# Performance work log

Hardware: AMD Instinct MI355X
Metric: run time of the kernel (lower is better)

Reference implementation:

```python
import jax, jax.numpy as jnp
import numpy as np

EMBED = 1024
HEADS = 16
HEAD_DIM = EMBED // HEADS


def setup_inputs() -> dict:
    key = jax.random.key(0)
    ks = jax.random.split(key, 9)
    s = 0.02
    return {
        "hidden_states": jax.random.normal(ks[0], (1, 4, 1500, EMBED), dtype=jnp.float32),
        "q_w": jax.random.normal(ks[1], (EMBED, EMBED), dtype=jnp.float32) * s,
        "q_b": jax.random.normal(ks[2], (EMBED,), dtype=jnp.float32) * s,
        "k_w": jax.random.normal(ks[3], (EMBED, EMBED), dtype=jnp.float32) * s,
        "v_w": jax.random.normal(ks[4], (EMBED, EMBED), dtype=jnp.float32) * s,
        "v_b": jax.random.normal(ks[5], (EMBED,), dtype=jnp.float32) * s,
        "out_w": jax.random.normal(ks[6], (EMBED, EMBED), dtype=jnp.float32) * s,
        "out_b": jax.random.normal(ks[7], (EMBED,), dtype=jnp.float32) * s,
    }


def reference(hidden_states, q_w, q_b, k_w, v_w, v_b, out_w, out_b):
    # hidden_states: [1, B, S, E]
    _, bsz, tgt_len, _ = hidden_states.shape
    x = hidden_states[0]  # [B, S, E]
    scaling = HEAD_DIM ** -0.5

    def split_heads(t):  # [B, S, E] -> [B, H, S, Dh]
        return t.reshape(bsz, tgt_len, HEADS, HEAD_DIM).transpose(0, 2, 1, 3)

    # Linear layers use torch convention: y = x @ W.T + b  (k_proj has no bias)
    q = split_heads((x @ q_w.T + q_b) * scaling)
    k = split_heads(x @ k_w.T)
    v = split_heads(x @ v_w.T + v_b)

    # attention scores [B, H, S, S]
    attn_weights = jnp.einsum("bhqd,bhkd->bhqk", q, k)
    attn_probs = jax.nn.softmax(attn_weights, axis=-1)
    attn_out = jnp.einsum("bhqk,bhkd->bhqd", attn_probs, v)  # [B, H, S, Dh]

    attn_out = attn_out.transpose(0, 2, 1, 3).reshape(1, bsz, tgt_len, EMBED)
    return attn_out @ out_w.T + out_b
```

## Files before the change

kernel.cpp:

```cpp
#include <hip/hip_runtime.h>
#include <cstddef>
#include <cstdint>

#define EMB 1024
#define SEQ 1500
#define NB 4
#define NH 16
#define DH 64
#define MTOT (NB*SEQ)
#define VTS 1536

typedef __bf16 bf16;
typedef __bf16 bf16x4 __attribute__((ext_vector_type(4)));
typedef __bf16 bf16x8 __attribute__((ext_vector_type(8)));
typedef short  s16x4  __attribute__((ext_vector_type(4)));
typedef float  f32x4  __attribute__((ext_vector_type(4)));

#define LOG2E 1.44269504088896340736f

__device__ __forceinline__ void async16(const void* g, const void* l) {
    __builtin_amdgcn_global_load_lds(
        (const __attribute__((address_space(1))) uint32_t*)g,
        (__attribute__((address_space(3))) uint32_t*)l, 16, 0, 0);
}

__device__ __forceinline__ uint32_t pack_bf16_trunc(float e0, float e1) {
    return __builtin_amdgcn_perm(__builtin_bit_cast(uint32_t, e1),
                                 __builtin_bit_cast(uint32_t, e0), 0x07060302u);
}

struct CvtArgs {
    const float* xs; bf16* xd;
    const float* w[4]; bf16* wd[4];
};

__global__ __launch_bounds__(256) void cvt_kernel(CvtArgs a) {
    const size_t NX = (size_t)MTOT * EMB;
    const size_t NW = (size_t)EMB * EMB;
    const size_t tot = NX + 4 * NW;
    for (size_t i = ((size_t)blockIdx.x * 256 + threadIdx.x) * 4; i < tot;
         i += (size_t)gridDim.x * 1024) {
        const float* s; bf16* d; size_t off;
        if (i < NX) { s = a.xs; d = a.xd; off = i; }
        else {
            size_t j = i - NX;
            int wi = (int)(j >> 20);
            off = j & (NW - 1);
            s = a.w[wi]; d = a.wd[wi];
        }
        float4 v = *(const float4*)(s + off);
        bf16x4 o = { (bf16)v.x, (bf16)v.y, (bf16)v.z, (bf16)v.w };
        *(bf16x4*)(d + off) = o;
    }
}

__global__ __launch_bounds__(256, 3) void gemm_fused(
    const bf16* __restrict__ X,
    const bf16* __restrict__ W0, const bf16* __restrict__ W1, const bf16* __restrict__ W2,
    const float* __restrict__ b_q, const float* __restrict__ b_v,
    bf16* __restrict__ Oq, bf16* __restrict__ Ok, bf16* __restrict__ Ovt,
    int M)
{
    __shared__ bf16 A0s[2][128 * 32];
    __shared__ bf16 A1s[2][128 * 32];
    __shared__ bf16 Bs [2][128 * 32];
    const int tid = threadIdx.x;
    const int lane = tid & 63, w = tid >> 6;
    const int q = lane >> 4, lr = lane & 15;
    const int wr = w >> 1, wc = w & 1;

    const int id = blockIdx.x;
    const bool isV = id >= 384;
    const int vid = isV ? id - 384 : id;
    const int mtile = (vid & 7) + ((vid >> 3) % 6) * 8;
    const int ntile = (vid >> 3) / 6;
    const int m0 = mtile * 128, n0 = ntile * 128;

    const int srow = w * 32 + (lane >> 2);
    const int swz_ch = (((lane & 3) ^ ((lane >> 3) & 3))) * 8;

    const bf16* pA0[2]; const bf16* pB[2];
    const size_t WOFF = (size_t)(W1 - W0);
#pragma unroll
    for (int i = 0; i < 2; i++) {
        int mr = m0 + srow + i * 16; mr = mr < M ? mr : M - 1;
        int nr = n0 + srow + i * 16;
        if (!isV) {
            pA0[i] = W0 + (size_t)nr * EMB + swz_ch;
            pB[i]  = X  + (size_t)mr * EMB + swz_ch;
        } else {
            pA0[i] = X  + (size_t)mr * EMB + swz_ch;
            pB[i]  = W2 + (size_t)nr * EMB + swz_ch;
        }
    }

#define STAGE(buf, off) do { \
    async16(pA0[0] + (off), A0s[buf] + (w * 2 + 0) * 512); \
    async16(pA0[1] + (off), A0s[buf] + (w * 2 + 1) * 512); \
    async16(pB[0]  + (off), Bs[buf]  + (w * 2 + 0) * 512); \
    async16(pB[1]  + (off), Bs[buf]  + (w * 2 + 1) * 512); \
    if (!isV) { \
        async16(pA0[0] + WOFF + (off), A1s[buf] + (w * 2 + 0) * 512); \
        async16(pA0[1] + WOFF + (off), A1s[buf] + (w * 2 + 1) * 512); } \
    } while (0)

    STAGE(0, 0);

    f32x4 acc0[4][4] = {};
    f32x4 acc1[4][4] = {};
    const int qsw = (q ^ ((lr >> 1) & 3)) * 8;
    const int arow = (wr * 64 + lr) * 32;
    const int brow = (wc * 64 + lr) * 32;

    for (int k0 = 0; k0 < EMB; k0 += 32) {
        const int cur = (k0 >> 5) & 1;
        __syncthreads();
        const int nxt = k0 + 32;
        if (nxt < EMB) STAGE(cur ^ 1, nxt);

        bf16x8 af[4], bfr[4];
#pragma unroll
        for (int t = 0; t < 4; t++) {
            bfr[t] = *(const bf16x8*)(Bs[cur]  + brow + t * 512 + qsw);
            af[t]  = *(const bf16x8*)(A0s[cur] + arow + t * 512 + qsw);
        }
#pragma unroll
        for (int ti = 0; ti < 4; ti++)
#pragma unroll
            for (int tj = 0; tj < 4; tj++)
                acc0[ti][tj] = __builtin_amdgcn_mfma_f32_16x16x32_bf16(
                    af[ti], bfr[tj], acc0[ti][tj], 0, 0, 0);
        if (!isV) {
#pragma unroll
            for (int t = 0; t < 4; t++)
                af[t] = *(const bf16x8*)(A1s[cur] + arow + t * 512 + qsw);
#pragma unroll
            for (int ti = 0; ti < 4; ti++)
#pragma unroll
                for (int tj = 0; tj < 4; tj++)
                    acc1[ti][tj] = __builtin_amdgcn_mfma_f32_16x16x32_bf16(
                        af[ti], bfr[tj], acc1[ti][tj], 0, 0, 0);
        }
    }
#undef STAGE

    if (!isV) {
        const float scale = 0.125f * LOG2E;
#pragma unroll
        for (int tj = 0; tj < 4; tj++) {
            const int m = m0 + wc * 64 + tj * 16 + lr;
            if (m >= M) continue;
            const int b_ = m / SEQ, s_ = m % SEQ;
#pragma unroll
            for (int ti = 0; ti < 4; ti++) {
                const int nb = n0 + wr * 64 + ti * 16 + q * 4;
                const int h = nb >> 6, d = nb & 63;
                const size_t ooff = (((size_t)b_ * NH + h) * SEQ + s_) * DH + d;
                const float4 b4 = *(const float4*)(b_q + nb);
                bf16x4 oq, ok;
                oq[0] = (bf16)((acc0[ti][tj][0] + b4.x) * scale);
                oq[1] = (bf16)((acc0[ti][tj][1] + b4.y) * scale);
                oq[2] = (bf16)((acc0[ti][tj][2] + b4.z) * scale);
                oq[3] = (bf16)((acc0[ti][tj][3] + b4.w) * scale);
                ok[0] = (bf16)(acc1[ti][tj][0]);
                ok[1] = (bf16)(acc1[ti][tj][1]);
                ok[2] = (bf16)(acc1[ti][tj][2]);
                ok[3] = (bf16)(acc1[ti][tj][3]);
                *(bf16x4*)(Oq + ooff) = oq;
                *(bf16x4*)(Ok + ooff) = ok;
            }
        }
    } else {
#pragma unroll
        for (int ti = 0; ti < 4; ti++) {
            const int mb = m0 + wr * 64 + ti * 16 + q * 4;
            if (mb >= M) continue;
            const int b_ = mb / SEQ, s_ = mb % SEQ;
#pragma unroll
            for (int tj = 0; tj < 4; tj++) {
                const int nb = n0 + wc * 64 + tj * 16 + lr;
                const int h = nb >> 6, d = nb & 63;
                const float bv = b_v[nb];
                bf16x4 o;
                o[0] = (bf16)(acc0[ti][tj][0] + bv);
                o[1] = (bf16)(acc0[ti][tj][1] + bv);
                o[2] = (bf16)(acc0[ti][tj][2] + bv);
                o[3] = (bf16)(acc0[ti][tj][3] + bv);
                *(bf16x4*)(Ovt + ((size_t)(b_ * NH + h) * DH + d) * VTS + s_) = o;
            }
        }
    }
}

__global__ __launch_bounds__(256) void gemm_out(
    const bf16* __restrict__ X, const bf16* __restrict__ Wo,
    const float* __restrict__ b_o, float* __restrict__ Of, int M)
{
    __shared__ bf16 As[2][128 * 32];
    __shared__ bf16 Bs[2][128 * 32];
    const int tid = threadIdx.x;
    const int lane = tid & 63, w = tid >> 6;
    const int q = lane >> 4, lr = lane & 15;
    const int wr = w >> 1, wc = w & 1;

    const int id = blockIdx.x;
    const int mtile = (id & 7) + ((id >> 3) % 6) * 8;
    const int ntile = (id >> 3) / 6;
    const int m0 = mtile * 128, n0 = ntile * 128;

    const int srow = w * 32 + (lane >> 2);
    const int swz_ch = (((lane & 3) ^ ((lane >> 3) & 3))) * 8;
    const bf16* pA[2]; const bf16* pB[2];
#pragma unroll
    for (int i = 0; i < 2; i++) {
        int ra = n0 + srow + i * 16;
        int rb = m0 + srow + i * 16; rb = rb < M ? rb : M - 1;
        pA[i] = Wo + (size_t)ra * EMB + swz_ch;
        pB[i] = X + (size_t)rb * EMB + swz_ch;
    }

#pragma unroll
    for (int i = 0; i < 2; i++) {
        async16(pA[i], As[0] + (w * 2 + i) * 512);
        async16(pB[i], Bs[0] + (w * 2 + i) * 512);
    }

    f32x4 acc[4][4] = {};
    const int qsw = (q ^ ((lr >> 1) & 3)) * 8;
    const int arow = (wr * 64 + lr) * 32;
    const int brow = (wc * 64 + lr) * 32;

    for (int k0 = 0; k0 < EMB; k0 += 32) {
        const int cur = (k0 >> 5) & 1;
        __syncthreads();
        const int nxt = k0 + 32;
        if (nxt < EMB) {
#pragma unroll
            for (int i = 0; i < 2; i++) {
                async16(pA[i] + nxt, As[cur ^ 1] + (w * 2 + i) * 512);
                async16(pB[i] + nxt, Bs[cur ^ 1] + (w * 2 + i) * 512);
            }
        }
        bf16x8 af[4], bfr[4];
#pragma unroll
        for (int t = 0; t < 4; t++) {
            af[t]  = *(const bf16x8*)(As[cur] + arow + t * 512 + qsw);
            bfr[t] = *(const bf16x8*)(Bs[cur] + brow + t * 512 + qsw);
        }
#pragma unroll
        for (int ti = 0; ti < 4; ti++)
#pragma unroll
            for (int tj = 0; tj < 4; tj++)
                acc[ti][tj] = __builtin_amdgcn_mfma_f32_16x16x32_bf16(
                    af[ti], bfr[tj], acc[ti][tj], 0, 0, 0);
    }

#pragma unroll
    for (int tj = 0; tj < 4; tj++) {
        const int m = m0 + wc * 64 + tj * 16 + lr;
        if (m >= M) continue;
#pragma unroll
        for (int ti = 0; ti < 4; ti++) {
            const int nb = n0 + wr * 64 + ti * 16 + q * 4;
            const float4 b4 = *(const float4*)(b_o + nb);
            float4 o;
            o.x = acc[ti][tj][0] + b4.x;
            o.y = acc[ti][tj][1] + b4.y;
            o.z = acc[ti][tj][2] + b4.z;
            o.w = acc[ti][tj][3] + b4.w;
            *(float4*)(Of + (size_t)m * EMB + nb) = o;
        }
    }
}

#define QG 3
__global__ __launch_bounds__(256) void attn_mfma(
    const bf16* __restrict__ Qb, const bf16* __restrict__ Kb,
    const bf16* __restrict__ Vt, bf16* __restrict__ ctx)
{
    __shared__ bf16 Ks[2][64 * 64];
    __shared__ bf16 Vs[2][64 * 64];
    const int tid = threadIdx.x;
    const int lane = tid & 63, w = tid >> 6;
    const int q = lane >> 4, lr = lane & 15;
    const int bh = blockIdx.x, b_ = bh >> 4, h_ = bh & 15;
    const int q0 = blockIdx.y * (QG * 64);
    const size_t base = (size_t)bh * SEQ * DH;
    const size_t vbase = (size_t)bh * DH * VTS;

    int qrow[QG];
    bf16x8 qf[QG][2];
#pragma unroll
    for (int g = 0; g < QG; g++) {
        qrow[g] = q0 + g * 64 + w * 16 + lr;
        const int qrc = qrow[g] < SEQ ? qrow[g] : (SEQ - 1);
        qf[g][0] = *(const bf16x8*)(Qb + base + (size_t)qrc * DH + q * 8);
        qf[g][1] = *(const bf16x8*)(Qb + base + (size_t)qrc * DH + 32 + q * 8);
    }

    f32x4 oacc[QG][4] = {};
    f32x4 lacc[QG] = {};
    const s16x4 ones = { (short)0x3F80, (short)0x3F80, (short)0x3F80, (short)0x3F80 };

    const int srow = tid >> 3;
    const int sch8 = ((tid & 7) ^ (srow & 7)) * 8;
    const int kswz = lr & 7;

    const int NT = (SEQ + 63) / 64;

    {
        int r0 = srow, r1 = srow + 32;
        async16(Kb + base + (size_t)r0 * DH + sch8, Ks[0] + tid * 8);
        async16(Kb + base + (size_t)r1 * DH + sch8, Ks[0] + tid * 8 + 2048);
        async16(Vt + vbase + (size_t)srow * VTS + sch8,        Vs[0] + tid * 8);
        async16(Vt + vbase + (size_t)(srow + 32) * VTS + sch8, Vs[0] + tid * 8 + 2048);
    }

    for (int kt = 0; kt < NT; kt++) {
        const int k0 = kt * 64;
        const int cur = kt & 1;
        __syncthreads();

        if (kt + 1 < NT) {
            const int kn = k0 + 64;
            int r0 = kn + srow;      if (r0 >= SEQ) r0 = SEQ - 1;
            int r1 = kn + srow + 32; if (r1 >= SEQ) r1 = SEQ - 1;
            async16(Kb + base + (size_t)r0 * DH + sch8, Ks[cur ^ 1] + tid * 8);
            async16(Kb + base + (size_t)r1 * DH + sch8, Ks[cur ^ 1] + tid * 8 + 2048);
            async16(Vt + vbase + (size_t)srow * VTS + kn + sch8,
                    Vs[cur ^ 1] + tid * 8);
            async16(Vt + vbase + (size_t)(srow + 32) * VTS + kn + sch8,
                    Vs[cur ^ 1] + tid * 8 + 2048);
        }

        const bf16* Kc = Ks[cur];
        const bf16* Vc = Vs[cur];

        bf16x8 kf[2][4];
#pragma unroll
        for (int s = 0; s < 2; s++)
#pragma unroll
            for (int mt = 0; mt < 4; mt++)
                kf[s][mt] = *(const bf16x8*)(Kc + (mt * 16 + lr) * 64 +
                                             ((4 * s + q) ^ kswz) * 8);

        s16x4 pf[QG][4];
#pragma unroll
        for (int g = 0; g < QG; g++) {
            f32x4 st[4] = {};
#pragma unroll
            for (int s = 0; s < 2; s++)
#pragma unroll
                for (int mt = 0; mt < 4; mt++)
                    st[mt] = __builtin_amdgcn_mfma_f32_16x16x32_bf16(
                        kf[s][mt], qf[g][s], st[mt], 0, 0, 0);

            if (k0 + 64 > SEQ) {
#pragma unroll
                for (int mt = 0; mt < 4; mt++)
#pragma unroll
                    for (int r = 0; r < 4; r++)
                        if (k0 + mt * 16 + q * 4 + r >= SEQ) st[mt][r] = -16384.0f;
            }

#pragma unroll
            for (int mt = 0; mt < 4; mt++) {
                float e0 = __builtin_amdgcn_exp2f(st[mt][0]);
                float e1 = __builtin_amdgcn_exp2f(st[mt][1]);
                float e2 = __builtin_amdgcn_exp2f(st[mt][2]);
                float e3 = __builtin_amdgcn_exp2f(st[mt][3]);
                uint32_t lo = pack_bf16_trunc(e0, e1);
                uint32_t hi = pack_bf16_trunc(e2, e3);
                uint2 pk = { lo, hi };
                pf[g][mt] = __builtin_bit_cast(s16x4, pk);
            }
#pragma unroll
            for (int c = 0; c < 4; c++)
                lacc[g] = __builtin_amdgcn_mfma_f32_16x16x16bf16_1k(
                    ones, pf[g][c], lacc[g], 0, 0, 0);
        }

#pragma unroll
        for (int c = 0; c < 4; c++) {
#pragma unroll
            for (int dt = 0; dt < 4; dt++) {
                const s16x4 vf = __builtin_bit_cast(s16x4,
                    *(const bf16x4*)(Vc + (dt * 16 + lr) * 64 +
                                     ((2 * c + (q >> 1)) ^ kswz) * 8 + (q & 1) * 4));
#pragma unroll
                for (int g = 0; g < QG; g++)
                    oacc[g][dt] = __builtin_amdgcn_mfma_f32_16x16x16bf16_1k(
                        vf, pf[g][c], oacc[g][dt], 0, 0, 0);
            }
        }
    }

#pragma unroll
    for (int g = 0; g < QG; g++) {
        const float inv = 1.0f / lacc[g][0];
        if (qrow[g] < SEQ) {
            const size_t rowoff = ((size_t)b_ * SEQ + qrow[g]) * EMB + h_ * DH;
#pragma unroll
            for (int dt = 0; dt < 4; dt++) {
                bf16x4 o;
#pragma unroll
                for (int r = 0; r < 4; r++) o[r] = (bf16)(oacc[g][dt][r] * inv);
                *(bf16x4*)(ctx + rowoff + dt * 16 + q * 4) = o;
            }
        }
    }
}

extern "C" void kernel_launch(void* const* d_in, const int* in_sizes, int n_in,
                              void* d_out, int out_size, void* d_ws, size_t ws_size,
                              hipStream_t stream) {
    const float* x     = (const float*)d_in[0];
    const float* q_w   = (const float*)d_in[1];
    const float* q_b   = (const float*)d_in[2];
    const float* k_w   = (const float*)d_in[3];
    const float* v_w   = (const float*)d_in[4];
    const float* v_b   = (const float*)d_in[5];
    const float* out_w = (const float*)d_in[6];
    const float* out_b = (const float*)d_in[7];
    float* out = (float*)d_out;

    const size_t nbuf = (size_t)MTOT * EMB;
    const size_t nvt  = (size_t)NB * NH * DH * VTS;
    const size_t nw   = (size_t)EMB * EMB;
    bf16* xb  = (bf16*)d_ws;
    bf16* qws = xb  + nbuf;
    bf16* kws = qws + nbuf;
    bf16* vtw = kws + nbuf;
    bf16* wqb = vtw + nvt;
    bf16* wkb = wqb + nw;
    bf16* wvb = wkb + nw;
    bf16* wob = wvb + nw;
    bf16* ctx = xb;

    CvtArgs ca;
    ca.xs = x;      ca.xd = xb;
    ca.w[0] = q_w;  ca.wd[0] = wqb;
    ca.w[1] = k_w;  ca.wd[1] = wkb;
    ca.w[2] = v_w;  ca.wd[2] = wvb;
    ca.w[3] = out_w; ca.wd[3] = wob;
    cvt_kernel<<<dim3(2560), 256, 0, stream>>>(ca);

    gemm_fused<<<dim3(768), 256, 0, stream>>>(
        xb, wqb, wkb, wvb, q_b, v_b, qws, kws, vtw, MTOT);

    attn_mfma<<<dim3(NB * NH, (SEQ + QG * 64 - 1) / (QG * 64)), 256, 0, stream>>>(
        qws, kws, vtw, ctx);

    gemm_out<<<dim3(384), 256, 0, stream>>>(ctx, wob, out_b, out, MTOT);
}
```

Baseline: 231.1 us.

## Fuse V projection into Q/K GEMM blocks sharing the X tile

Each block of the fused projection GEMM now computes Q, K and V for the same 128x128 tile, staging all three weight tiles and reusing a single X tile, instead of running separate V-only blocks. This cuts the grid from 768 to 384 blocks and removes the redundant reloading of X for the V projection. The price is a third accumulator set and extra shared memory per block, so launch bounds drop to 2 blocks per CU. V is now written as four scalar strided stores per fragment instead of one vectorized bf16x4 store.

```diff
diff --git a/kernel.cpp b/kernel.cpp
--- a/kernel.cpp
+++ b/kernel.cpp
@@ -54,7 +54,7 @@
     }
 }
 
-__global__ __launch_bounds__(256, 3) void gemm_fused(
+__global__ __launch_bounds__(256, 2) void gemm_fused(
     const bf16* __restrict__ X,
     const bf16* __restrict__ W0, const bf16* __restrict__ W1, const bf16* __restrict__ W2,
     const float* __restrict__ b_q, const float* __restrict__ b_v,
@@ -63,6 +63,7 @@
 {
     __shared__ bf16 A0s[2][128 * 32];
     __shared__ bf16 A1s[2][128 * 32];
+    __shared__ bf16 A2s[2][128 * 32];
     __shared__ bf16 Bs [2][128 * 32];
     const int tid = threadIdx.x;
     const int lane = tid & 63, w = tid >> 6;
@@ -70,44 +71,40 @@
     const int wr = w >> 1, wc = w & 1;
 
     const int id = blockIdx.x;
-    const bool isV = id >= 384;
-    const int vid = isV ? id - 384 : id;
-    const int mtile = (vid & 7) + ((vid >> 3) % 6) * 8;
-    const int ntile = (vid >> 3) / 6;
+    const int mtile = (id & 7) + ((id >> 3) % 6) * 8;
+    const int ntile = (id >> 3) / 6;
     const int m0 = mtile * 128, n0 = ntile * 128;
 
     const int srow = w * 32 + (lane >> 2);
     const int swz_ch = (((lane & 3) ^ ((lane >> 3) & 3))) * 8;
 
-    const bf16* pA0[2]; const bf16* pB[2];
-    const size_t WOFF = (size_t)(W1 - W0);
+    const bf16* pA[2]; const bf16* pB[2];
+    const size_t WOFF1 = (size_t)(W1 - W0);
+    const size_t WOFF2 = (size_t)(W2 - W0);
 #pragma unroll
     for (int i = 0; i < 2; i++) {
+        int nr = n0 + srow + i * 16;
         int mr = m0 + srow + i * 16; mr = mr < M ? mr : M - 1;
-        int nr = n0 + srow + i * 16;
-        if (!isV) {
-            pA0[i] = W0 + (size_t)nr * EMB + swz_ch;
-            pB[i]  = X  + (size_t)mr * EMB + swz_ch;
-        } else {
-            pA0[i] = X  + (size_t)mr * EMB + swz_ch;
-            pB[i]  = W2 + (size_t)nr * EMB + swz_ch;
-        }
+        pA[i] = W0 + (size_t)nr * EMB + swz_ch;
+        pB[i] = X  + (size_t)mr * EMB + swz_ch;
     }
 
 #define STAGE(buf, off) do { \
-    async16(pA0[0] + (off), A0s[buf] + (w * 2 + 0) * 512); \
-    async16(pA0[1] + (off), A0s[buf] + (w * 2 + 1) * 512); \
-    async16(pB[0]  + (off), Bs[buf]  + (w * 2 + 0) * 512); \
-    async16(pB[1]  + (off), Bs[buf]  + (w * 2 + 1) * 512); \
-    if (!isV) { \
-        async16(pA0[0] + WOFF + (off), A1s[buf] + (w * 2 + 0) * 512); \
-        async16(pA0[1] + WOFF + (off), A1s[buf] + (w * 2 + 1) * 512); } \
+    async16(pA[0] + (off),         A0s[buf] + (w * 2 + 0) * 512); \
+    async16(pA[1] + (off),         A0s[buf] + (w * 2 + 1) * 512); \
+    async16(pA[0] + WOFF1 + (off), A1s[buf] + (w * 2 + 0) * 512); \
+    async16(pA[1] + WOFF1 + (off), A1s[buf] + (w * 2 + 1) * 512); \
+    async16(pA[0] + WOFF2 + (off), A2s[buf] + (w * 2 + 0) * 512); \
+    async16(pA[1] + WOFF2 + (off), A2s[buf] + (w * 2 + 1) * 512); \
+    async16(pB[0] + (off),         Bs[buf]  + (w * 2 + 0) * 512); \
+    async16(pB[1] + (off),         Bs[buf]  + (w * 2 + 1) * 512); \
     } while (0)
 
     STAGE(0, 0);
 
     f32x4 acc0[4][4] = {};
     f32x4 acc1[4][4] = {};
+    f32x4 acc2[4][4] = {};
     const int qsw = (q ^ ((lr >> 1) & 3)) * 8;
     const int arow = (wr * 64 + lr) * 32;
     const int brow = (wc * 64 + lr) * 32;
@@ -130,64 +127,56 @@
             for (int tj = 0; tj < 4; tj++)
                 acc0[ti][tj] = __builtin_amdgcn_mfma_f32_16x16x32_bf16(
                     af[ti], bfr[tj], acc0[ti][tj], 0, 0, 0);
-        if (!isV) {
-#pragma unroll
-            for (int t = 0; t < 4; t++)
-                af[t] = *(const bf16x8*)(A1s[cur] + arow + t * 512 + qsw);
-#pragma unroll
-            for (int ti = 0; ti < 4; ti++)
-#pragma unroll
-                for (int tj = 0; tj < 4; tj++)
-                    acc1[ti][tj] = __builtin_amdgcn_mfma_f32_16x16x32_bf16(
-                        af[ti], bfr[tj], acc1[ti][tj], 0, 0, 0);
-        }
+#pragma unroll
+        for (int t = 0; t < 4; t++)
+            af[t] = *(const bf16x8*)(A1s[cur] + arow + t * 512 + qsw);
+#pragma unroll
+        for (int ti = 0; ti < 4; ti++)
+#pragma unroll
+            for (int tj = 0; tj < 4; tj++)
+                acc1[ti][tj] = __builtin_amdgcn_mfma_f32_16x16x32_bf16(
+                    af[ti], bfr[tj], acc1[ti][tj], 0, 0, 0);
+#pragma unroll
+        for (int t = 0; t < 4; t++)
+            af[t] = *(const bf16x8*)(A2s[cur] + arow + t * 512 + qsw);
+#pragma unroll
+        for (int ti = 0; ti < 4; ti++)
+#pragma unroll
+            for (int tj = 0; tj < 4; tj++)
+                acc2[ti][tj] = __builtin_amdgcn_mfma_f32_16x16x32_bf16(
+                    af[ti], bfr[tj], acc2[ti][tj], 0, 0, 0);
     }
 #undef STAGE
 
-    if (!isV) {
-        const float scale = 0.125f * LOG2E;
-#pragma unroll
-        for (int tj = 0; tj < 4; tj++) {
-            const int m = m0 + wc * 64 + tj * 16 + lr;
-            if (m >= M) continue;
-            const int b_ = m / SEQ, s_ = m % SEQ;
-#pragma unroll
-            for (int ti = 0; ti < 4; ti++) {
-                const int nb = n0 + wr * 64 + ti * 16 + q * 4;
-                const int h = nb >> 6, d = nb & 63;
-                const size_t ooff = (((size_t)b_ * NH + h) * SEQ + s_) * DH + d;
-                const float4 b4 = *(const float4*)(b_q + nb);
-                bf16x4 oq, ok;
-                oq[0] = (bf16)((acc0[ti][tj][0] + b4.x) * scale);
-                oq[1] = (bf16)((acc0[ti][tj][1] + b4.y) * scale);
-                oq[2] = (bf16)((acc0[ti][tj][2] + b4.z) * scale);
-                oq[3] = (bf16)((acc0[ti][tj][3] + b4.w) * scale);
-                ok[0] = (bf16)(acc1[ti][tj][0]);
-                ok[1] = (bf16)(acc1[ti][tj][1]);
-                ok[2] = (bf16)(acc1[ti][tj][2]);
-                ok[3] = (bf16)(acc1[ti][tj][3]);
-                *(bf16x4*)(Oq + ooff) = oq;
-                *(bf16x4*)(Ok + ooff) = ok;
-            }
-        }
-    } else {
+    const float scale = 0.125f * LOG2E;
+#pragma unroll
+    for (int tj = 0; tj < 4; tj++) {
+        const int m = m0 + wc * 64 + tj * 16 + lr;
+        if (m >= M) continue;
+        const int b_ = m / SEQ, s_ = m % SEQ;
 #pragma unroll
         for (int ti = 0; ti < 4; ti++) {
-            const int mb = m0 + wr * 64 + ti * 16 + q * 4;
-            if (mb >= M) continue;
-            const int b_ = mb / SEQ, s_ = mb % SEQ;
-#pragma unroll
-            for (int tj = 0; tj < 4; tj++) {
-                const int nb = n0 + wc * 64 + tj * 16 + lr;
-                const int h = nb >> 6, d = nb & 63;
-                const float bv = b_v[nb];
-                bf16x4 o;
-                o[0] = (bf16)(acc0[ti][tj][0] + bv);
-                o[1] = (bf16)(acc0[ti][tj][1] + bv);
-                o[2] = (bf16)(acc0[ti][tj][2] + bv);
-                o[3] = (bf16)(acc0[ti][tj][3] + bv);
-                *(bf16x4*)(Ovt + ((size_t)(b_ * NH + h) * DH + d) * VTS + s_) = o;
-            }
+            const int nb = n0 + wr * 64 + ti * 16 + q * 4;
+            const int h = nb >> 6, d = nb & 63;
+            const size_t ooff = (((size_t)b_ * NH + h) * SEQ + s_) * DH + d;
+            const float4 b4 = *(const float4*)(b_q + nb);
+            bf16x4 oq, ok;
+            oq[0] = (bf16)((acc0[ti][tj][0] + b4.x) * scale);
+            oq[1] = (bf16)((acc0[ti][tj][1] + b4.y) * scale);
+            oq[2] = (bf16)((acc0[ti][tj][2] + b4.z) * scale);
+            oq[3] = (bf16)((acc0[ti][tj][3] + b4.w) * scale);
+            ok[0] = (bf16)(acc1[ti][tj][0]);
+            ok[1] = (bf16)(acc1[ti][tj][1]);
+            ok[2] = (bf16)(acc1[ti][tj][2]);
+            ok[3] = (bf16)(acc1[ti][tj][3]);
+            *(bf16x4*)(Oq + ooff) = oq;
+            *(bf16x4*)(Ok + ooff) = ok;
+            const float4 bv = *(const float4*)(b_v + nb);
+            bf16* vp = Ovt + ((size_t)(b_ * NH + h) * DH + d) * VTS + s_;
+            vp[0]           = (bf16)(acc2[ti][tj][0] + bv.x);
+            vp[VTS]         = (bf16)(acc2[ti][tj][1] + bv.y);
+            vp[2 * VTS]     = (bf16)(acc2[ti][tj][2] + bv.z);
+            vp[3 * VTS]     = (bf16)(acc2[ti][tj][3] + bv.w);
         }
     }
 }
@@ -445,7 +434,7 @@
     ca.w[3] = out_w; ca.wd[3] = wob;
     cvt_kernel<<<dim3(2560), 256, 0, stream>>>(ca);
 
-    gemm_fused<<<dim3(768), 256, 0, stream>>>(
+    gemm_fused<<<dim3(384), 256, 0, stream>>>(
         xb, wqb, wkb, wvb, q_b, v_b, qws, kws, vtw, MTOT);
 
     attn_mfma<<<dim3(NB * NH, (SEQ + QG * 64 - 1) / (QG * 64)), 256, 0, stream>>>(
```

Result: no change. 232.3 us (+0.5%).
